# Performance work log

Measured on AMD Instinct MI355X. Metric: run time of the kernel, lower is better.

Reference implementation:

```python
import jax, jax.numpy as jnp
import numpy as np

D_MODEL = 1024
D_FF = 4096
BATCH = 4
SEQ = 2048
DECAY = 0.9
THRESH = 0.5


def setup_inputs() -> dict:
    key = jax.random.key(0)
    k1, k2, k3, k4 = jax.random.split(key, 4)
    spikes = jax.random.normal(k1, (BATCH, SEQ, D_MODEL), dtype=jnp.float32)
    # xavier-ish init scales matching gains 0.5/0.5/0.3 in the torch module
    s1 = 0.5 * np.sqrt(2.0 / (D_MODEL + D_FF))
    s2 = 0.5 * np.sqrt(2.0 / (D_MODEL + D_FF))
    sr = 0.3 * np.sqrt(2.0 / (D_MODEL + D_FF))
    W1 = jax.random.normal(k2, (D_FF, D_MODEL), dtype=jnp.float32) * s1
    W2 = jax.random.normal(k3, (D_MODEL, D_FF), dtype=jnp.float32) * s2
    Wr = jax.random.normal(k4, (D_FF, D_MODEL), dtype=jnp.float32) * sr
    return {"spikes": spikes, "W1": W1, "W2": W2, "Wr": Wr}


def reference(spikes, W1, W2, Wr):
    # spikes: [B, T, D]; W1, Wr: [F, D]; W2: [D, F]
    B, T, D = spikes.shape
    F = W1.shape[0]
    d = jnp.float32(DECAY)
    one_minus_d = jnp.float32(1.0 - DECAY)
    # Hoist time-independent projections out of the recurrence (same math as
    # the per-timestep nn.Linear calls in the torch loop).
    r_all = jax.nn.sigmoid(jnp.einsum('btd,fd->btf', spikes, Wr))  # [B,T,F]
    h_all = jnp.einsum('btd,fd->btf', spikes, W1)                   # [B,T,F]

    def step(carry, xs):
        act, rec = carry              # [B,F] each, init zeros (fresh buffers)
        r_t, h_t = xs                 # [B,F]
        rec = d * rec + one_minus_d * r_t                 # mixed receptance
        mixed = d * act + one_minus_d * h_t               # temporal state mix
        spike = (mixed > THRESH).astype(h_t.dtype)        # eval-mode spikes
        gated = spike * r_t
        # torch detaches current_activation each step
        return (jax.lax.stop_gradient(mixed), rec), gated

    init = (jnp.zeros((B, F), spikes.dtype), jnp.zeros((B, F), spikes.dtype))
    _, gated = jax.lax.scan(step,
                            init,
                            (jnp.swapaxes(r_all, 0, 1), jnp.swapaxes(h_all, 0, 1)))
    # gated: [T, B, F] -> output [B, T, D]
    out = jnp.einsum('tbf,df->btd', gated, W2)
    return out
```

## Files before the change

kernel.cpp:

```cpp
#include <hip/hip_runtime.h>
#include <math.h>

#define B_    4
#define T_    2048
#define D_    1024
#define F_    4096
#define R_    (B_*T_)
#define SEG_  64
#define L_    (T_/SEG_)
#define DECAYF 0.9f
#define OMDF   0.1f
#define FLAG_THRESH 0.45f


typedef __attribute__((ext_vector_type(4)))  int   i32x4;
typedef __attribute__((ext_vector_type(8)))  int   i32x8;
typedef __attribute__((ext_vector_type(16))) float f32x16;

__device__ __forceinline__ int pk_fp8x4(float x, float y, float z, float w) {
    int p = 0;
    p = __builtin_amdgcn_cvt_pk_fp8_f32(x, y, p, false);
    p = __builtin_amdgcn_cvt_pk_fp8_f32(z, w, p, true);
    return p;
}

__device__ __forceinline__ size_t pk_off(int row, int d) {
    return ((size_t)((row >> 5) * 16 + (d >> 6)) * 2048)
         + ((d >> 4) & 1) * 1024
         + ((row & 31) + ((d >> 5) & 1) * 32) * 16
         + (d & 15);
}

#define KA_W1_BLOCKS  4096
#define KA_SEG_BLOCKS 256
#define KA_FLAG_BLOCKS 32

__global__ __launch_bounds__(256)
void kA_prologue(const float* __restrict__ spikes,
                 const float* __restrict__ W1,
                 unsigned char* __restrict__ w_f8,
                 float* __restrict__ seg_sum,
                 unsigned int* __restrict__ flags) {
    const int bid = blockIdx.x;
    const int tid = threadIdx.x;
    if (bid < KA_W1_BLOCKS) {
        int i = bid * 256 + tid;
        float4 v = ((const float4*)W1)[i];
        int f  = i >> 8;
        int d0 = (i & 255) * 4;
        *(int*)(w_f8 + pk_off(f, d0)) = pk_fp8x4(8.f*v.x, 8.f*v.y, 8.f*v.z, 8.f*v.w);
    } else if (bid < KA_W1_BLOCKS + KA_SEG_BLOCKS) {
        int t = (bid - KA_W1_BLOCKS) * 256 + tid;
        int dg = t & (D_ / 4 - 1);
        int s = (t >> 8) & (SEG_ - 1);
        int b = t >> 14;
        const float4* sp4 = (const float4*)spikes;
        const int base = (b * T_ + s * L_) * (D_ / 4) + dg;
        float4 e = {0.f, 0.f, 0.f, 0.f};
#pragma unroll 8
        for (int k = 0; k < L_; ++k) {
            float4 x = sp4[base + k * (D_ / 4)];
            e.x = DECAYF * e.x + OMDF * x.x;
            e.y = DECAYF * e.y + OMDF * x.y;
            e.z = DECAYF * e.z + OMDF * x.z;
            e.w = DECAYF * e.w + OMDF * x.w;
        }
        ((float4*)seg_sum)[(b * SEG_ + s) * (D_ / 4) + dg] = e;
    } else {
        int i = (bid - KA_W1_BLOCKS - KA_SEG_BLOCKS) * 256 + tid;
        if (i < R_) flags[i] = 0u;
    }
}

__global__ __launch_bounds__(256)
void kB_seg_scan(const float* __restrict__ seg_sum,
                 float* __restrict__ start_state) {
    int g = blockIdx.x * 256 + threadIdx.x;
    int s = g & 63;
    int c = g >> 6;
    int d = c & (D_ - 1);
    int b = c >> 10;
    int idx = (b * SEG_ + s) * D_ + d;
    float v = seg_sum[idx];
    float wp = 0.0343368382f;
#pragma unroll
    for (int off = 1; off < SEG_; off <<= 1) {
        float u = __shfl_up(v, off, 64);
        if (s >= off) v += wp * u;
        wp *= wp;
    }
    float pv = __shfl_up(v, 1, 64);
    start_state[idx] = (s == 0) ? 0.f : pv;
}

__global__ __launch_bounds__(256)
void kC_ema_fp8(const float* __restrict__ spikes,
                const float* __restrict__ start_state,
                unsigned char* __restrict__ a_f8) {
    int t = blockIdx.x * 256 + threadIdx.x;
    int dg = t & (D_ / 4 - 1);
    int s = (t >> 8) & (SEG_ - 1);
    int b = t >> 14;
    const float4* sp4 = (const float4*)spikes;
    const int base = (b * T_ + s * L_) * (D_ / 4) + dg;
    const int d0 = dg * 4;
    unsigned char* dst = a_f8 + pk_off(b * T_ + s * L_, d0);
    float4 e = ((const float4*)start_state)[(b * SEG_ + s) * (D_ / 4) + dg];
#pragma unroll 8
    for (int k = 0; k < L_; ++k) {
        float4 x = sp4[base + k * (D_ / 4)];
        e.x = DECAYF * e.x + OMDF * x.x;
        e.y = DECAYF * e.y + OMDF * x.y;
        e.z = DECAYF * e.z + OMDF * x.z;
        e.w = DECAYF * e.w + OMDF * x.w;
        *(int*)(dst + k * 16) = pk_fp8x4(8.f*e.x, 8.f*e.y, 8.f*e.z, 8.f*e.w);
    }
}

__global__ __launch_bounds__(256)
void k2_mfma_flags(const unsigned char* __restrict__ Ap,
                   const unsigned char* __restrict__ Bp,
                   unsigned int* __restrict__ flags) {
    const int tid = threadIdx.x;
    const int w = tid >> 6;
    const int lane = tid & 63;
    const int orig = blockIdx.x;
    const int swz  = (orig & 7) * 128 + (orig >> 3);
    const int m0 = (swz >> 4) * 128;
    const int n0 = (swz & 15) * 256;
    const int wm = w >> 1, wn = w & 1;
    const int kg = lane >> 5;

    const unsigned char* a0 = Ap + ((size_t)((m0 >> 5) + wm * 2 + 0) * 16) * 2048 + lane * 16;
    const unsigned char* a1 = Ap + ((size_t)((m0 >> 5) + wm * 2 + 1) * 16) * 2048 + lane * 16;
    const unsigned char* b0 = Bp + ((size_t)((n0 >> 5) + wn * 4 + 0) * 16) * 2048 + lane * 16;
    const unsigned char* b1 = Bp + ((size_t)((n0 >> 5) + wn * 4 + 1) * 16) * 2048 + lane * 16;
    const unsigned char* b2 = Bp + ((size_t)((n0 >> 5) + wn * 4 + 2) * 16) * 2048 + lane * 16;
    const unsigned char* b3 = Bp + ((size_t)((n0 >> 5) + wn * 4 + 3) * 16) * 2048 + lane * 16;

    f32x16 acc[2][4] = {};

#define LDF(p, OFF)                                                         \
    ({ i32x4 lo_ = *(const i32x4*)((p) + (OFF));                            \
       i32x4 hi_ = *(const i32x4*)((p) + (OFF) + 1024);                     \
       (i32x8){lo_.x, lo_.y, lo_.z, lo_.w, hi_.x, hi_.y, hi_.z, hi_.w}; })

#define MFMA1(i, j, AF, BF)                                                 \
    acc[i][j] = __builtin_amdgcn_mfma_scale_f32_32x32x64_f8f6f4(            \
        AF, BF, acc[i][j], 0, 0, 0, 124, 0, 124);

#define MFMA8(S)                                                            \
    MFMA1(0, 0, A0##S, B0##S) MFMA1(0, 1, A0##S, B1##S)                     \
    MFMA1(0, 2, A0##S, B2##S) MFMA1(0, 3, A0##S, B3##S)                     \
    MFMA1(1, 0, A1##S, B0##S) MFMA1(1, 1, A1##S, B1##S)                     \
    MFMA1(1, 2, A1##S, B2##S) MFMA1(1, 3, A1##S, B3##S)

#define LOADSTAGE(S, OFF)                                                   \
    A0##S = LDF(a0, OFF); A1##S = LDF(a1, OFF);                             \
    B0##S = LDF(b0, OFF); B1##S = LDF(b1, OFF);                             \
    B2##S = LDF(b2, OFF); B3##S = LDF(b3, OFF);

    i32x8 A0s0, A1s0, B0s0, B1s0, B2s0, B3s0;
    i32x8 A0s1, A1s1, B0s1, B1s1, B2s1, B3s1;
    i32x8 A0s2, A1s2, B0s2, B1s2, B2s2, B3s2;
    i32x8 A0s3, A1s3, B0s3, B1s3, B2s3, B3s3;
    LOADSTAGE(s0, 0)
    LOADSTAGE(s1, 2048)
    LOADSTAGE(s2, 4096)
    LOADSTAGE(s3, 6144)

#pragma unroll 1
    for (int p = 0; p < 3; ++p) {
        const size_t off = (size_t)(p + 1) * 8192;
        MFMA8(s0)
        LOADSTAGE(s0, off)
        MFMA8(s1)
        LOADSTAGE(s1, off + 2048)
        MFMA8(s2)
        LOADSTAGE(s2, off + 4096)
        MFMA8(s3)
        LOADSTAGE(s3, off + 6144)
    }
    MFMA8(s0)
    MFMA8(s1)
    MFMA8(s2)
    MFMA8(s3)
#undef LDF
#undef MFMA1
#undef MFMA8
#undef LOADSTAGE

#pragma unroll
    for (int i = 0; i < 2; ++i) {
#pragma unroll
        for (int reg = 0; reg < 16; ++reg) {
            float mx = fmaxf(fmaxf(acc[i][0][reg], acc[i][1][reg]),
                             fmaxf(acc[i][2][reg], acc[i][3][reg]));
            if (mx > FLAG_THRESH) {
                const int rr = (reg & 3) + 8 * (reg >> 2) + 4 * kg;
                atomicOr(&flags[m0 + wm * 64 + i * 32 + rr], 1u);
            }
        }
    }
}

__global__ __launch_bounds__(256)
void k4_output(const float* __restrict__ spikes,
               const float* __restrict__ start_state,
               const float* __restrict__ W1,
               const float* __restrict__ Wr,
               const float* __restrict__ W2,
               const unsigned int* __restrict__ flags,
               float* __restrict__ out) {
    const int row = blockIdx.x;
    const int tid = threadIdx.x;
    float4 o = {0.f, 0.f, 0.f, 0.f};

    if (flags[row] == 0u) {
        *(float4*)&out[(size_t)row * D_ + tid * 4] = o;
        return;
    }

    __shared__ float se[D_];
    __shared__ float sp[D_];
    __shared__ float red[256];
    __shared__ int nspk;
    __shared__ int spk_list[256];

    const int b = row / T_;
    const int t = row % T_;
    const int seg = t / L_;
    const int off = t % L_;
    const int segbase = (b * T_ + seg * L_) * D_;

    for (int i = tid; i < D_; i += 256) {
        float e = start_state[(b * SEG_ + seg) * D_ + i];
        for (int j = 0; j <= off; ++j)
            e = DECAYF * e + OMDF * spikes[segbase + j * D_ + i];
        se[i] = e;
        sp[i] = spikes[(size_t)row * D_ + i];
    }
    if (tid == 0) nspk = 0;
    __syncthreads();

    for (int f0 = 0; f0 < F_; f0 += 256) {
        int f = f0 + tid;
        float mix = 0.f;
        for (int k = 0; k < D_; ++k) mix += se[k] * W1[(size_t)f * D_ + k];
        if (mix > 0.5f) {
            int idx = atomicAdd(&nspk, 1);
            spk_list[idx] = f;
        }
        __syncthreads();
        int n = nspk;
        for (int i = 0; i < n; ++i) {
            int fs = spk_list[i];
            float part = 0.f;
#pragma unroll
            for (int k = 0; k < 4; ++k)
                part += sp[tid * 4 + k] * Wr[(size_t)fs * D_ + tid * 4 + k];
            red[tid] = part;
            __syncthreads();
            for (int sft = 128; sft > 0; sft >>= 1) {
                if (tid < sft) red[tid] += red[tid + sft];
                __syncthreads();
            }
            float r = 1.f / (1.f + expf(-red[0]));
            __syncthreads();
            o.x += r * W2[(size_t)(tid * 4 + 0) * F_ + fs];
            o.y += r * W2[(size_t)(tid * 4 + 1) * F_ + fs];
            o.z += r * W2[(size_t)(tid * 4 + 2) * F_ + fs];
            o.w += r * W2[(size_t)(tid * 4 + 3) * F_ + fs];
        }
        __syncthreads();
        if (tid == 0) nspk = 0;
        __syncthreads();
    }
    *(float4*)&out[(size_t)row * D_ + tid * 4] = o;
}

extern "C" void kernel_launch(void* const* d_in, const int* in_sizes, int n_in,
                              void* d_out, int out_size, void* d_ws, size_t ws_size,
                              hipStream_t stream) {
    const float* spikes = (const float*)d_in[0];
    const float* W1     = (const float*)d_in[1];
    const float* W2     = (const float*)d_in[2];
    const float* Wr     = (const float*)d_in[3];
    float* out = (float*)d_out;

    char* ws = (char*)d_ws;
    float* seg_sum      = (float*)ws;
    float* start_state  = seg_sum + (size_t)B_ * SEG_ * D_;
    unsigned int* flags = (unsigned int*)(start_state + (size_t)B_ * SEG_ * D_);
    unsigned char* a_f8 = (unsigned char*)(flags + R_);
    unsigned char* w_f8 = a_f8 + (size_t)R_ * D_;

    kA_prologue<<<KA_W1_BLOCKS + KA_SEG_BLOCKS + KA_FLAG_BLOCKS, 256, 0, stream>>>(
        spikes, W1, w_f8, seg_sum, flags);
    kB_seg_scan<<<(B_ * D_ * 64) / 256, 256, 0, stream>>>(seg_sum, start_state);
    kC_ema_fp8<<<(B_ * SEG_ * D_ / 4) / 256, 256, 0, stream>>>(spikes, start_state, a_f8);

    k2_mfma_flags<<<(R_ / 128) * (F_ / 256), 256, 0, stream>>>(a_f8, w_f8, flags);

    k4_output<<<R_, 256, 0, stream>>>(spikes, start_state, W1, Wr, W2, flags, out);
}
```

Measured before the change: 174.3 us.

## Stage FP8 packed tiles in LDS for coalesced writes and remap GEMM tiles per XCD

The W1 FP8 conversion and the EMA FP8 conversion now write their packed 32-row tiles into a swizzled 32 KB shared-memory buffer first. Each block then copies the buffer to global memory as contiguous 16-byte stores, which replaces the scattered 4-byte writes. The GEMM block-to-tile mapping is also changed so that each XCD covers a contiguous 2D region of M and N tiles, aiming for better L2 reuse. In exchange, the W1 conversion runs on only 128 blocks with 32 KB of LDS each, which lowers parallelism in that part of the prologue.

```diff
diff --git a/kernel.cpp b/kernel.cpp
--- a/kernel.cpp
+++ b/kernel.cpp
@@ -31,7 +31,11 @@
          + (d & 15);
 }
 
-#define KA_W1_BLOCKS  4096
+__device__ __forceinline__ int lsw(int o) {
+    return o ^ (((o >> 9) & 7) << 4);
+}
+
+#define KA_W1_BLOCKS  128
 #define KA_SEG_BLOCKS 256
 #define KA_FLAG_BLOCKS 32
 
@@ -43,12 +47,25 @@
                  unsigned int* __restrict__ flags) {
     const int bid = blockIdx.x;
     const int tid = threadIdx.x;
+    __shared__ unsigned char stage[32768];
     if (bid < KA_W1_BLOCKS) {
-        int i = bid * 256 + tid;
-        float4 v = ((const float4*)W1)[i];
-        int f  = i >> 8;
-        int d0 = (i & 255) * 4;
-        *(int*)(w_f8 + pk_off(f, d0)) = pk_fp8x4(8.f*v.x, 8.f*v.y, 8.f*v.z, 8.f*v.w);
+        const int d0 = tid * 4;
+        const int lbase = (d0 >> 6) * 2048 + ((d0 >> 4) & 1) * 1024
+                        + ((d0 >> 5) & 1) * 512 + (d0 & 15);
+        const float4* w4 = (const float4*)W1 + (size_t)bid * 32 * 256 + tid;
+#pragma unroll 8
+        for (int r = 0; r < 32; ++r) {
+            float4 v = w4[(size_t)r * 256];
+            *(int*)&stage[lsw(lbase + r * 16)] =
+                pk_fp8x4(8.f*v.x, 8.f*v.y, 8.f*v.z, 8.f*v.w);
+        }
+        __syncthreads();
+        i32x4* dst = (i32x4*)(w_f8 + (size_t)bid * 32768);
+#pragma unroll
+        for (int r = 0; r < 8; ++r) {
+            const int byte = (r * 256 + tid) * 16;
+            dst[r * 256 + tid] = *(const i32x4*)&stage[lsw(byte)];
+        }
     } else if (bid < KA_W1_BLOCKS + KA_SEG_BLOCKS) {
         int t = (bid - KA_W1_BLOCKS) * 256 + tid;
         int dg = t & (D_ / 4 - 1);
@@ -97,15 +114,16 @@
 void kC_ema_fp8(const float* __restrict__ spikes,
                 const float* __restrict__ start_state,
                 unsigned char* __restrict__ a_f8) {
-    int t = blockIdx.x * 256 + threadIdx.x;
-    int dg = t & (D_ / 4 - 1);
-    int s = (t >> 8) & (SEG_ - 1);
-    int b = t >> 14;
+    const int bs = blockIdx.x;
+    const int b = bs >> 6, s = bs & 63;
+    const int tid = threadIdx.x;
+    const int d0 = tid * 4;
+    __shared__ unsigned char stage[32768];
+    const int lbase = (d0 >> 6) * 2048 + ((d0 >> 4) & 1) * 1024
+                    + ((d0 >> 5) & 1) * 512 + (d0 & 15);
     const float4* sp4 = (const float4*)spikes;
-    const int base = (b * T_ + s * L_) * (D_ / 4) + dg;
-    const int d0 = dg * 4;
-    unsigned char* dst = a_f8 + pk_off(b * T_ + s * L_, d0);
-    float4 e = ((const float4*)start_state)[(b * SEG_ + s) * (D_ / 4) + dg];
+    const int base = (b * T_ + s * L_) * (D_ / 4) + tid;
+    float4 e = ((const float4*)start_state)[bs * (D_ / 4) + tid];
 #pragma unroll 8
     for (int k = 0; k < L_; ++k) {
         float4 x = sp4[base + k * (D_ / 4)];
@@ -113,7 +131,15 @@
         e.y = DECAYF * e.y + OMDF * x.y;
         e.z = DECAYF * e.z + OMDF * x.z;
         e.w = DECAYF * e.w + OMDF * x.w;
-        *(int*)(dst + k * 16) = pk_fp8x4(8.f*e.x, 8.f*e.y, 8.f*e.z, 8.f*e.w);
+        *(int*)&stage[lsw(lbase + k * 16)] =
+            pk_fp8x4(8.f*e.x, 8.f*e.y, 8.f*e.z, 8.f*e.w);
+    }
+    __syncthreads();
+    i32x4* dst = (i32x4*)(a_f8 + (size_t)bs * 32768);
+#pragma unroll
+    for (int r = 0; r < 8; ++r) {
+        const int byte = (r * 256 + tid) * 16;
+        dst[r * 256 + tid] = *(const i32x4*)&stage[lsw(byte)];
     }
 }
 
@@ -125,9 +151,12 @@
     const int w = tid >> 6;
     const int lane = tid & 63;
     const int orig = blockIdx.x;
-    const int swz  = (orig & 7) * 128 + (orig >> 3);
-    const int m0 = (swz >> 4) * 128;
-    const int n0 = (swz & 15) * 256;
+    const int xcd  = orig & 7;
+    const int id   = orig >> 3;
+    const int mt   = (xcd >> 1) * 16 + (id >> 3);
+    const int nt   = (xcd & 1) * 8 + (id & 7);
+    const int m0 = mt * 128;
+    const int n0 = nt * 256;
     const int wm = w >> 1, wn = w & 1;
     const int kg = lane >> 5;
 
@@ -298,7 +327,7 @@
     kA_prologue<<<KA_W1_BLOCKS + KA_SEG_BLOCKS + KA_FLAG_BLOCKS, 256, 0, stream>>>(
         spikes, W1, w_f8, seg_sum, flags);
     kB_seg_scan<<<(B_ * D_ * 64) / 256, 256, 0, stream>>>(seg_sum, start_state);
-    kC_ema_fp8<<<(B_ * SEG_ * D_ / 4) / 256, 256, 0, stream>>>(spikes, start_state, a_f8);
+    kC_ema_fp8<<<B_ * SEG_, 256, 0, stream>>>(spikes, start_state, a_f8);
 
     k2_mfma_flags<<<(R_ / 128) * (F_ / 256), 256, 0, stream>>>(a_f8, w_f8, flags);
 
```

Measured after the change: 165.0 us. 5.3% less time.
